# Performance work log

Hardware: AMD Instinct MI355X
Metric: run time of the kernel (lower is better)

The kernel has to match this reference:

```python
import jax, jax.numpy as jnp
import numpy as np
from jax import lax

B, L, M, H = 8, 16, 256, 53
HID, NH, HD = 64, 4, 16  # hidden_size, n_heads, head_dim
ACT = 15  # 3 sub-actions x 5 categories


def _lstm_last(x, Wih, Whh, bih, bhh):
    # x: [N, T, D] batch_first; torch LSTM gate order i,f,g,o. Returns last hidden [N, HID].
    N = x.shape[0]
    h0 = jnp.zeros((N, HID), x.dtype)
    c0 = jnp.zeros((N, HID), x.dtype)
    def step(carry, xt):
        h, c = carry
        g = xt @ Wih.T + bih + h @ Whh.T + bhh
        i, f, gg, o = jnp.split(g, 4, axis=-1)
        c = jax.nn.sigmoid(f) * c + jax.nn.sigmoid(i) * jnp.tanh(gg)
        h = jax.nn.sigmoid(o) * jnp.tanh(c)
        return (h, c), None
    (h, _), _ = lax.scan(step, (h0, c0), x.transpose(1, 0, 2))
    return h


def setup_inputs():
    key = jax.random.key(0)
    ks = jax.random.split(key, 32)
    rn = lambda k, sh: (jax.random.normal(k, sh, jnp.float32) * 0.05)
    Gmat = jax.random.randint(ks[3], (M, M), 0, 2)
    Gmat = Gmat.at[jnp.arange(M), jnp.arange(M)].set(1)  # self-contact so no all-masked row
    return {
        'x_actor': jax.random.normal(ks[0], (B, L, M, H), jnp.float32),
        'x_critic': jax.random.normal(ks[1], (B, L, M, H), jnp.float32),
        'action': jax.random.randint(ks[2], (B, M, 3), 0, 5),
        'Gmat': Gmat,
        'Wa': rn(ks[4], (HID, H)), 'ba': jnp.zeros((HID,), jnp.float32),
        'Wg': rn(ks[5], (HID, H)), 'bg': jnp.zeros((HID,), jnp.float32),
        'Qw': rn(ks[6], (HID, HID)), 'Kw': rn(ks[7], (HID, HID)),
        'W2': rn(ks[8], (HID, 2 * HID)), 'b2': jnp.zeros((HID,), jnp.float32),
        'Wih_a': rn(ks[9], (4 * HID, HID)), 'Whh_a': rn(ks[10], (4 * HID, HID)),
        'bih_a': jnp.zeros((4 * HID,), jnp.float32), 'bhh_a': jnp.zeros((4 * HID,), jnp.float32),
        'Wih_c': rn(ks[11], (4 * HID, HID)), 'Whh_c': rn(ks[12], (4 * HID, HID)),
        'bih_c': jnp.zeros((4 * HID,), jnp.float32), 'bhh_c': jnp.zeros((4 * HID,), jnp.float32),
        'Wma1': rn(ks[13], (HID, HID)), 'bma1': jnp.zeros((HID,), jnp.float32),
        'Wma2': rn(ks[14], (ACT, HID)), 'bma2': jnp.zeros((ACT,), jnp.float32),
        'Wmc1': rn(ks[15], (HID, HID)), 'bmc1': jnp.zeros((HID,), jnp.float32),
        'Wmc2': rn(ks[16], (1, HID)), 'bmc2': jnp.zeros((1,), jnp.float32),
    }


def reference(x_actor, x_critic, action, Gmat, Wa, ba, Wg, bg, Qw, Kw, W2, b2,
              Wih_a, Whh_a, bih_a, bhh_a, Wih_c, Whh_c, bih_c, bhh_c,
              Wma1, bma1, Wma2, bma2, Wmc1, bmc1, Wmc2, bmc2):
    Bb, Ll, Mm, Hh = x_actor.shape
    xa = x_actor.transpose(1, 0, 2, 3).reshape(Ll * Bb, Mm, Hh)
    xc = xa  # original code overwrites x_critic with x_actor (preserved)
    a_lin = xa @ Wa.T + ba                               # [LB, M, HID]
    # --- GAT (GCN2) ---
    s = xc @ Wg.T + bg                                   # [LB, M, HID]
    q = (s @ Qw).reshape(-1, Mm, NH, HD)
    k = (s @ Kw).reshape(-1, Mm, NH, HD)
    s4 = s.reshape(-1, Mm, NH, HD)
    att = jnp.einsum('blhe,bshe->bhls', q, k) / jnp.asarray(128.0, s.dtype) ** 0.5
    att = jnp.where(Gmat > 0, att, jnp.asarray(-9e15, att.dtype))
    att = jax.nn.softmax(att, axis=-1)
    s_out = jnp.einsum('bshe,bhls->blhe', s4, att).reshape(-1, Mm, NH * HD)
    c_feat = jnp.concatenate([s, s_out], axis=-1) @ W2.T + b2  # [LB, M, HID]
    # --- to sequences [B*M, L, HID] ---
    xa_seq = a_lin.reshape(Ll, Bb * Mm, HID).transpose(1, 0, 2)
    xc_seq = c_feat.reshape(Ll, Bb * Mm, HID).transpose(1, 0, 2)
    ah = _lstm_last(xa_seq, Wih_a, Whh_a, bih_a, bhh_a)          # [B*M, HID]
    ch = _lstm_last(xc_seq, Wih_c, Whh_c, bih_c, bhh_c).reshape(Bb, Mm, HID)
    logits = (jnp.tanh(ah @ Wma1.T + bma1) @ Wma2.T + bma2).reshape(Bb, Mm, 3, 5)
    logp = jax.nn.log_softmax(logits, axis=-1)
    lp = jnp.take_along_axis(logp, action[..., None], axis=-1).squeeze(-1)  # [B,M,3]
    ent = -jnp.sum(jnp.exp(logp) * logp, axis=-1)                           # [B,M,3]
    value = jnp.tanh(ch @ Wmc1.T + bmc1) @ Wmc2.T + bmc2                    # [B,M,1]
    return (action, lp.sum(-1), ent.sum(-1), value)
```

## Files before the change

kernel.cpp:

```cpp
#include <hip/hip_runtime.h>
#include <math.h>

#define B_ 8
#define L_ 16
#define M_ 256
#define H_ 53
#define HID_ 64
#define LB_ 128
#define SCALE_ 0.08838834764831845f

typedef __attribute__((ext_vector_type(8))) short bf16x8;
typedef __attribute__((ext_vector_type(4))) float f32x4;

__device__ inline unsigned short f2bf(float f) {
  unsigned u = __builtin_bit_cast(unsigned, f);
  unsigned r = (u + 0x7FFFu + ((u >> 16) & 1u)) >> 16;
  return (unsigned short)r;
}
__device__ inline float bf2f(unsigned short u) {
  unsigned v = ((unsigned)u) << 16;
  return __builtin_bit_cast(float, v);
}
__device__ inline float sigm(float x) { return __builtin_amdgcn_rcpf(1.f + __expf(-x)); }
__device__ inline float ftanh(float x) { return 1.f - 2.f * __builtin_amdgcn_rcpf(1.f + __expf(2.f * x)); }

__global__ __launch_bounds__(256) void kP_pre(
    const float* __restrict__ Wg, const float* __restrict__ bg,
    const float* __restrict__ Qw, const float* __restrict__ Kw,
    unsigned short* __restrict__ WQ_b, unsigned short* __restrict__ WK_b,
    float* __restrict__ bqk) {
  int blk = blockIdx.x, tid = threadIdx.x;
  if (blk < 32) {
    int idx = blk * 256 + tid;
    int which = idx >> 12, n = (idx >> 6) & 63, j = idx & 63;
    const float* Mm = which ? Kw : Qw;
    float acc = 0.f;
    if (j < 53) {
      for (int e = 0; e < 64; ++e) acc = fmaf(Mm[e * 64 + n], Wg[e * 53 + j], acc);
      if (which == 0) acc *= SCALE_;
    }
    (which ? WK_b : WQ_b)[n * 64 + j] = f2bf(acc);
  } else {
    if (tid < 128) {
      int which = tid >> 6, n = tid & 63;
      const float* Mm = which ? Kw : Qw;
      float acc = 0.f;
      for (int e = 0; e < 64; ++e) acc = fmaf(bg[e], Mm[e * 64 + n], acc);
      if (which == 0) acc *= SCALE_;
      bqk[tid] = acc;
    }
  }
}

#define XS 68
#define WS 68
#define OS 268
__global__ __launch_bounds__(256, 2) void kA_lin(const float* __restrict__ x,
    const float* __restrict__ Wa, const float* __restrict__ ba,
    const float* __restrict__ Wg, const float* __restrict__ bg,
    const unsigned short* __restrict__ WQ_b, const unsigned short* __restrict__ WK_b,
    const float* __restrict__ bqk,
    const int* __restrict__ Gmat, const float* __restrict__ Wih_c,
    const float* __restrict__ W2, const float* __restrict__ b2,
    const float* __restrict__ Whh_a, const float* __restrict__ Whh_c,
    const float* __restrict__ Wih_a,
    unsigned short* __restrict__ a_lin_bf, unsigned short* __restrict__ s_b,
    unsigned short* __restrict__ q_b, unsigned short* __restrict__ k_b,
    unsigned short* __restrict__ sT_b,
    unsigned short* __restrict__ Wfold_b, float* __restrict__ bias_fold,
    unsigned* __restrict__ gmask,
    unsigned short* __restrict__ Whha_b, unsigned short* __restrict__ Whhc_b,
    unsigned short* __restrict__ Wiha_b) {
  int blk = blockIdx.x, tid = threadIdx.x;
  if (blk >= 512) {
    int b2k = blk - 512;
    if (b2k < 128) {
      int idx = b2k * 256 + tid;
      int n = idx >> 7, t = idx & 127;
      float acc = 0.f;
      for (int e = 0; e < 64; ++e) acc = fmaf(Wih_c[n * 64 + e], W2[e * 128 + t], acc);
      Wfold_b[idx] = f2bf(acc);
    } else if (b2k < 192) {
      int l = (b2k - 128) * 4 + (tid >> 6);
      int ln = tid & 63;
      #pragma unroll
      for (int c = 0; c < 4; ++c) {
        int gv = Gmat[l * 256 + c * 64 + ln];
        unsigned long long msk = __ballot(gv > 0);
        if (ln == 0) {
          gmask[l * 8 + c * 2] = (unsigned)msk;
          gmask[l * 8 + c * 2 + 1] = (unsigned)(msk >> 32);
        }
      }
    } else if (b2k == 192) {
      float acc = 0.f;
      for (int e = 0; e < 64; ++e) acc = fmaf(Wih_c[tid * 64 + e], b2[e], acc);
      bias_fold[tid] = acc;
    } else {
      int base = (b2k - 193) * 2048;
      #pragma unroll
      for (int k = 0; k < 8; ++k) {
        int idx = base + k * 256 + tid;
        if (idx < 16384) Whha_b[idx] = f2bf(Whh_a[idx]);
        else if (idx < 32768) Whhc_b[idx - 16384] = f2bf(Whh_c[idx - 16384]);
        else Wiha_b[idx - 32768] = f2bf(Wih_a[idx - 32768]);
      }
    }
    return;
  }
  __shared__ __attribute__((aligned(16))) unsigned short x_lds[64 * XS];
  __shared__ __attribute__((aligned(16))) unsigned short w_lds[256 * WS];
  __shared__ float bias_lds[256];
  __shared__ __attribute__((aligned(16))) unsigned short out_lds[64 * OS];
  int row0 = blk * 64;
  for (int i = tid; i < 64 * 64; i += 256) {
    int r = i >> 6, j = i & 63;
    int row = row0 + r;
    int lb = row >> 8, m = row & 255;
    int l = lb >> 3, b = lb & 7;
    float v = (j < 53) ? x[((b * L_ + l) * M_ + m) * H_ + j] : 0.f;
    x_lds[r * XS + j] = f2bf(v);
  }
  for (int i = tid; i < 64 * 64; i += 256) {
    int n = i >> 6, j = i & 63;
    w_lds[n * WS + j] = (j < 53) ? f2bf(Wa[n * 53 + j]) : 0;
    w_lds[(64 + n) * WS + j] = (j < 53) ? f2bf(Wg[n * 53 + j]) : 0;
    w_lds[(128 + n) * WS + j] = WQ_b[i];
    w_lds[(192 + n) * WS + j] = WK_b[i];
  }
  {
    float bv;
    if (tid < 64) bv = ba[tid];
    else if (tid < 128) bv = bg[tid - 64];
    else bv = bqk[tid - 128];
    bias_lds[tid] = bv;
  }
  __syncthreads();
  int lane = tid & 63, w = tid >> 6;
  int c16 = lane & 15, q4 = lane >> 4;
  bf16x8 a0 = *(const bf16x8*)&x_lds[(w * 16 + c16) * XS + q4 * 8];
  bf16x8 a1 = *(const bf16x8*)&x_lds[(w * 16 + c16) * XS + 32 + q4 * 8];
  #pragma unroll
  for (int nt = 0; nt < 16; ++nt) {
    bf16x8 b0 = *(const bf16x8*)&w_lds[(nt * 16 + c16) * WS + q4 * 8];
    bf16x8 b1 = *(const bf16x8*)&w_lds[(nt * 16 + c16) * WS + 32 + q4 * 8];
    float bs = bias_lds[nt * 16 + c16];
    f32x4 acc = {bs, bs, bs, bs};
    acc = __builtin_amdgcn_mfma_f32_16x16x32_bf16(a0, b0, acc, 0, 0, 0);
    acc = __builtin_amdgcn_mfma_f32_16x16x32_bf16(a1, b1, acc, 0, 0, 0);
    #pragma unroll
    for (int rr = 0; rr < 4; ++rr)
      out_lds[(w * 16 + q4 * 4 + rr) * OS + nt * 16 + c16] = f2bf(acc[rr]);
  }
  __syncthreads();
  for (int i = tid; i < 2048; i += 256) {
    int r = i >> 5, seg = i & 31;
    int which = seg >> 3, n8 = (seg & 7) * 8;
    uint4 v = *(const uint4*)&out_lds[r * OS + which * 64 + n8];
    unsigned short* dst = which == 0 ? a_lin_bf : which == 1 ? s_b : which == 2 ? q_b : k_b;
    *(uint4*)&dst[(row0 + r) * 64 + n8] = v;
  }
  int lbA = row0 >> 8, m0 = row0 & 255;
  for (int i = tid; i < 1024; i += 256) {
    int e = i >> 4, mc = i & 15;
    ushort4 v;
    v.x = out_lds[(mc * 4 + 0) * OS + 64 + e];
    v.y = out_lds[(mc * 4 + 1) * OS + 64 + e];
    v.z = out_lds[(mc * 4 + 2) * OS + 64 + e];
    v.w = out_lds[(mc * 4 + 3) * OS + 64 + e];
    *(ushort4*)&sT_b[(lbA * 64 + e) * 256 + m0 + mc * 4] = v;
  }
}

__global__ __launch_bounds__(512, 4) void kB_attn(
    const unsigned short* __restrict__ qb, const unsigned short* __restrict__ kb,
    const unsigned short* __restrict__ sT, const unsigned* __restrict__ gmask,
    unsigned short* __restrict__ so_b) {
  __shared__ __attribute__((aligned(16))) unsigned short k_lds[256 * 68];
  __shared__ __attribute__((aligned(16))) unsigned short sT_lds[64 * 280];
  int blk = blockIdx.x;
  int lb = blk >> 2;
  int l0 = (blk & 3) << 6;
  int tid = threadIdx.x;
  int kbase = lb * 256;
  for (int i = tid; i < 2048; i += 512) {
    int s = i >> 3, e8 = (i & 7) * 8;
    *(uint4*)&k_lds[s * 68 + e8] = *(const uint4*)(kb + (kbase + s) * 64 + e8);
  }
  for (int i = tid; i < 2048; i += 512) {
    int e = i >> 5, m8 = (i & 31) * 8;
    *(uint4*)&sT_lds[e * 280 + m8] = *(const uint4*)(sT + (lb * 64 + e) * 256 + m8);
  }
  int lane = tid & 63, w = tid >> 6;
  int c16 = lane & 15, q4 = lane >> 4;
  int lrow0 = (w >> 1) * 16;
  int h0 = (w & 1) * 2;
  int lrow = lb * 256 + l0 + lrow0;
  const bf16x8 z8 = {0, 0, 0, 0, 0, 0, 0, 0};
  bf16x8 bq[2];
  #pragma unroll
  for (int hp = 0; hp < 2; ++hp) {
    int h = h0 + hp;
    bq[hp] = (q4 < 2) ? *(const bf16x8*)(qb + (lrow + c16) * 64 + h * 16 + q4 * 8) : z8;
  }
  unsigned gwv[8];
  #pragma unroll
  for (int sp = 0; sp < 8; ++sp) gwv[sp] = gmask[(l0 + lrow0 + c16) * 8 + sp];
  __syncthreads();
  f32x4 accO[2];
  float sumh[2];
  #pragma unroll
  for (int hp = 0; hp < 2; ++hp) { accO[hp] = (f32x4){0.f, 0.f, 0.f, 0.f}; sumh[hp] = 0.f; }

  #pragma unroll
  for (int sp = 0; sp < 8; ++sp) {
    unsigned gw = gwv[sp];
    #pragma unroll
    for (int hp = 0; hp < 2; ++hp) {
      int h = h0 + hp;
      unsigned pk0A, pk1A, pk0B, pk1B;
      #pragma unroll
      for (int tp = 0; tp < 2; ++tp) {
        int t = sp * 2 + tp;
        bf16x8 ka = z8;
        if (q4 < 2) ka = *(const bf16x8*)&k_lds[(t * 16 + c16) * 68 + h * 16 + q4 * 8];
        f32x4 d = __builtin_amdgcn_mfma_f32_16x16x32_bf16(ka, bq[hp], (f32x4){0.f, 0.f, 0.f, 0.f}, 0, 0, 0);
        int bitbase = tp * 16 + q4 * 4;
        float p0 = ((gw >> (bitbase + 0)) & 1u) ? __expf(d[0]) : 0.f;
        float p1 = ((gw >> (bitbase + 1)) & 1u) ? __expf(d[1]) : 0.f;
        float p2 = ((gw >> (bitbase + 2)) & 1u) ? __expf(d[2]) : 0.f;
        float p3 = ((gw >> (bitbase + 3)) & 1u) ? __expf(d[3]) : 0.f;
        sumh[hp] += (p0 + p1) + (p2 + p3);
        unsigned lo = (unsigned)f2bf(p0) | ((unsigned)f2bf(p1) << 16);
        unsigned hi = (unsigned)f2bf(p2) | ((unsigned)f2bf(p3) << 16);
        if (tp == 0) { pk0A = lo; pk1A = hi; } else { pk0B = lo; pk1B = hi; }
      }
      int srcA = ((q4 & 1) * 2) * 16 + c16, srcB = srcA + 16;
      unsigned g0A = (unsigned)__shfl((int)pk0A, srcA);
      unsigned g1A = (unsigned)__shfl((int)pk1A, srcA);
      unsigned g2A = (unsigned)__shfl((int)pk0A, srcB);
      unsigned g3A = (unsigned)__shfl((int)pk1A, srcB);
      unsigned g0B = (unsigned)__shfl((int)pk0B, srcA);
      unsigned g1B = (unsigned)__shfl((int)pk1B, srcA);
      unsigned g2B = (unsigned)__shfl((int)pk0B, srcB);
      unsigned g3B = (unsigned)__shfl((int)pk1B, srcB);
      bool useB = (q4 >= 2);
      uint4 av;
      av.x = useB ? g0B : g0A;
      av.y = useB ? g1B : g1A;
      av.z = useB ? g2B : g2A;
      av.w = useB ? g3B : g3A;
      bf16x8 af = __builtin_bit_cast(bf16x8, av);
      bf16x8 bs = *(const bf16x8*)&sT_lds[(h * 16 + c16) * 280 + sp * 32 + q4 * 8];
      accO[hp] = __builtin_amdgcn_mfma_f32_16x16x32_bf16(af, bs, accO[hp], 0, 0, 0);
    }
  }
  #pragma unroll
  for (int hp = 0; hp < 2; ++hp) {
    int h = h0 + hp;
    float s = sumh[hp];
    s += __shfl_xor(s, 16);
    s += __shfl_xor(s, 32);
    #pragma unroll
    for (int r = 0; r < 4; ++r) {
      float sv = __shfl(s, q4 * 4 + r);
      float o = accO[hp][r] / sv;
      so_b[(lb * 256 + l0 + lrow0 + q4 * 4 + r) * 64 + h * 16 + c16] = f2bf(o);
    }
  }
}

__global__ __launch_bounds__(256, 1) void kR_lstm(
    const unsigned short* __restrict__ a_lin_bf,
    const unsigned short* __restrict__ s_b, const unsigned short* __restrict__ so_b,
    const unsigned short* __restrict__ Wfold_b, const float* __restrict__ bias_fold,
    const unsigned short* __restrict__ Wiha_b,
    const unsigned short* __restrict__ Whha_b, const unsigned short* __restrict__ Whhc_b,
    const float* __restrict__ bih_a, const float* __restrict__ bhh_a,
    const float* __restrict__ bih_c, const float* __restrict__ bhh_c,
    const int* __restrict__ action,
    const float* __restrict__ Wma1, const float* __restrict__ bma1,
    const float* __restrict__ Wma2, const float* __restrict__ bma2,
    const float* __restrict__ Wmc1, const float* __restrict__ bmc1,
    const float* __restrict__ Wmc2, const float* __restrict__ bmc2,
    float* __restrict__ out) {
  int blk = blockIdx.x;
  int which = blk >> 7, g = blk & 127;
  int seq0 = g * 16;
  int b = seq0 >> 8, m0 = seq0 & 255;
  __shared__ __attribute__((aligned(16))) unsigned short h_lds[2][16][72];
  __shared__ __attribute__((aligned(16))) unsigned short ha_lds[16][72];
  __shared__ float logit_lds[16][16];
  __shared__ float grp_lds[16][8];
  __shared__ float val_lds[16][4];
  int tid = threadIdx.x;
  int lane = tid & 63, w = tid >> 6;
  int c16 = lane & 15, q4 = lane >> 4;
  int hs0 = w * 16;
  const unsigned short* Whh_b = which ? Whhc_b : Whha_b;
  const float* bih = which ? bih_c : bih_a;
  const float* bhh = which ? bhh_c : bhh_a;
  bf16x8 bwhh[4][2];
  float bias[4];
  #pragma unroll
  for (int nt = 0; nt < 4; ++nt) {
    int n = nt * 64 + hs0 + c16;
    bias[nt] = bih[n] + bhh[n] + (which ? bias_fold[n] : 0.f);
    #pragma unroll
    for (int kf = 0; kf < 2; ++kf)
      bwhh[nt][kf] = *(const bf16x8*)(Whh_b + n * 64 + kf * 32 + q4 * 8);
  }
  for (int i = tid; i < 576; i += 256) ((unsigned*)h_lds)[i] = 0u;
  float cr[4] = {0.f, 0.f, 0.f, 0.f};
  const int STEP = 2048 * 64;
  __syncthreads();
  int cur = 0;
  if (which == 0) {
    bf16x8 bwin[4][2];
    #pragma unroll
    for (int nt = 0; nt < 4; ++nt) {
      int n = nt * 64 + hs0 + c16;
      #pragma unroll
      for (int kf = 0; kf < 2; ++kf)
        bwin[nt][kf] = *(const bf16x8*)(Wiha_b + n * 64 + kf * 32 + q4 * 8);
    }
    const unsigned short* inb = a_lin_bf + (b * 256 + m0 + c16) * 64;
    bf16x8 i0c = *(const bf16x8*)(inb + q4 * 8);
    bf16x8 i1c = *(const bf16x8*)(inb + 32 + q4 * 8);
    for (int l = 0; l < L_; ++l) {
      bf16x8 i0n = i0c, i1n = i1c;
      if (l < L_ - 1) {
        i0n = *(const bf16x8*)(inb + (l + 1) * STEP + q4 * 8);
        i1n = *(const bf16x8*)(inb + (l + 1) * STEP + 32 + q4 * 8);
      }
      bf16x8 ah0 = *(const bf16x8*)&h_lds[cur][c16][q4 * 8];
      bf16x8 ah1 = *(const bf16x8*)&h_lds[cur][c16][32 + q4 * 8];
      f32x4 acc[4];
      #pragma unroll
      for (int nt = 0; nt < 4; ++nt) {
        f32x4 a = {bias[nt], bias[nt], bias[nt], bias[nt]};
        a = __builtin_amdgcn_mfma_f32_16x16x32_bf16(i0c, bwin[nt][0], a, 0, 0, 0);
        a = __builtin_amdgcn_mfma_f32_16x16x32_bf16(i1c, bwin[nt][1], a, 0, 0, 0);
        a = __builtin_amdgcn_mfma_f32_16x16x32_bf16(ah0, bwhh[nt][0], a, 0, 0, 0);
        a = __builtin_amdgcn_mfma_f32_16x16x32_bf16(ah1, bwhh[nt][1], a, 0, 0, 0);
        acc[nt] = a;
      }
      #pragma unroll
      for (int rr = 0; rr < 4; ++rr) {
        float si = sigm(acc[0][rr]);
        float sf = sigm(acc[1][rr]);
        float gg = ftanh(acc[2][rr]);
        float so_ = sigm(acc[3][rr]);
        cr[rr] = sf * cr[rr] + si * gg;
        float hvv = so_ * ftanh(cr[rr]);
        h_lds[cur ^ 1][q4 * 4 + rr][hs0 + c16] = f2bf(hvv);
      }
      __syncthreads();
      cur ^= 1;
      i0c = i0n; i1c = i1n;
    }
  } else {
    bf16x8 bwf[4][4];
    #pragma unroll
    for (int nt = 0; nt < 4; ++nt) {
      int n = nt * 64 + hs0 + c16;
      #pragma unroll
      for (int kc = 0; kc < 4; ++kc)
        bwf[nt][kc] = *(const bf16x8*)(Wfold_b + n * 128 + kc * 32 + q4 * 8);
    }
    const unsigned short* sbB = s_b + (b * 256 + m0 + c16) * 64;
    const unsigned short* soB = so_b + (b * 256 + m0 + c16) * 64;
    bf16x8 s0c = *(const bf16x8*)(sbB + q4 * 8);
    bf16x8 s1c = *(const bf16x8*)(sbB + 32 + q4 * 8);
    bf16x8 o0c = *(const bf16x8*)(soB + q4 * 8);
    bf16x8 o1c = *(const bf16x8*)(soB + 32 + q4 * 8);
    for (int l = 0; l < L_; ++l) {
      bf16x8 s0n = s0c, s1n = s1c, o0n = o0c, o1n = o1c;
      if (l < L_ - 1) {
        s0n = *(const bf16x8*)(sbB + (l + 1) * STEP + q4 * 8);
        s1n = *(const bf16x8*)(sbB + (l + 1) * STEP + 32 + q4 * 8);
        o0n = *(const bf16x8*)(soB + (l + 1) * STEP + q4 * 8);
        o1n = *(const bf16x8*)(soB + (l + 1) * STEP + 32 + q4 * 8);
      }
      bf16x8 ah0 = *(const bf16x8*)&h_lds[cur][c16][q4 * 8];
      bf16x8 ah1 = *(const bf16x8*)&h_lds[cur][c16][32 + q4 * 8];
      f32x4 acc[4];
      #pragma unroll
      for (int nt = 0; nt < 4; ++nt) {
        f32x4 a = {bias[nt], bias[nt], bias[nt], bias[nt]};
        a = __builtin_amdgcn_mfma_f32_16x16x32_bf16(s0c, bwf[nt][0], a, 0, 0, 0);
        a = __builtin_amdgcn_mfma_f32_16x16x32_bf16(s1c, bwf[nt][1], a, 0, 0, 0);
        a = __builtin_amdgcn_mfma_f32_16x16x32_bf16(o0c, bwf[nt][2], a, 0, 0, 0);
        a = __builtin_amdgcn_mfma_f32_16x16x32_bf16(o1c, bwf[nt][3], a, 0, 0, 0);
        a = __builtin_amdgcn_mfma_f32_16x16x32_bf16(ah0, bwhh[nt][0], a, 0, 0, 0);
        a = __builtin_amdgcn_mfma_f32_16x16x32_bf16(ah1, bwhh[nt][1], a, 0, 0, 0);
        acc[nt] = a;
      }
      #pragma unroll
      for (int rr = 0; rr < 4; ++rr) {
        float si = sigm(acc[0][rr]);
        float sf = sigm(acc[1][rr]);
        float gg = ftanh(acc[2][rr]);
        float so_ = sigm(acc[3][rr]);
        cr[rr] = sf * cr[rr] + si * gg;
        float hvv = so_ * ftanh(cr[rr]);
        h_lds[cur ^ 1][q4 * 4 + rr][hs0 + c16] = f2bf(hvv);
      }
      __syncthreads();
      cur ^= 1;
      s0c = s0n; s1c = s1n; o0c = o0n; o1c = o1n;
    }
  }
  bf16x8 fh0 = *(const bf16x8*)&h_lds[cur][c16][q4 * 8];
  bf16x8 fh1 = *(const bf16x8*)&h_lds[cur][c16][32 + q4 * 8];
  if (which == 0) {
    bf16x8 bm1[2];
    #pragma unroll
    for (int kf = 0; kf < 2; ++kf) {
      const float* wp = Wma1 + (hs0 + c16) * 64 + kf * 32 + q4 * 8;
      bf16x8 bb;
      #pragma unroll
      for (int j = 0; j < 8; ++j) bb[j] = (short)f2bf(wp[j]);
      bm1[kf] = bb;
    }
    float bs = bma1[hs0 + c16];
    f32x4 acc = {bs, bs, bs, bs};
    acc = __builtin_amdgcn_mfma_f32_16x16x32_bf16(fh0, bm1[0], acc, 0, 0, 0);
    acc = __builtin_amdgcn_mfma_f32_16x16x32_bf16(fh1, bm1[1], acc, 0, 0, 0);
    #pragma unroll
    for (int rr = 0; rr < 4; ++rr)
      ha_lds[q4 * 4 + rr][hs0 + c16] = f2bf(ftanh(acc[rr]));
    __syncthreads();
    if (w == 0) {
      bf16x8 af0 = *(const bf16x8*)&ha_lds[c16][q4 * 8];
      bf16x8 af1 = *(const bf16x8*)&ha_lds[c16][32 + q4 * 8];
      const bf16x8 z8 = {0, 0, 0, 0, 0, 0, 0, 0};
      bf16x8 bw2[2] = {z8, z8};
      float bs2 = 0.f;
      if (c16 < 15) {
        #pragma unroll
        for (int kf = 0; kf < 2; ++kf) {
          const float* wp = Wma2 + c16 * 64 + kf * 32 + q4 * 8;
          bf16x8 bb;
          #pragma unroll
          for (int j = 0; j < 8; ++j) bb[j] = (short)f2bf(wp[j]);
          bw2[kf] = bb;
        }
        bs2 = bma2[c16];
      }
      f32x4 acc2 = {bs2, bs2, bs2, bs2};
      acc2 = __builtin_amdgcn_mfma_f32_16x16x32_bf16(af0, bw2[0], acc2, 0, 0, 0);
      acc2 = __builtin_amdgcn_mfma_f32_16x16x32_bf16(af1, bw2[1], acc2, 0, 0, 0);
      #pragma unroll
      for (int rr = 0; rr < 4; ++rr)
        logit_lds[q4 * 4 + rr][c16] = acc2[rr];
    }
    __syncthreads();
    if (tid < 48) {
      int useq = tid & 15, t = tid >> 4;
      int n = seq0 + useq;
      float l0 = logit_lds[useq][t * 5 + 0], l1 = logit_lds[useq][t * 5 + 1];
      float l2 = logit_lds[useq][t * 5 + 2], l3 = logit_lds[useq][t * 5 + 3];
      float l4 = logit_lds[useq][t * 5 + 4];
      float mx = fmaxf(fmaxf(fmaxf(l0, l1), fmaxf(l2, l3)), l4);
      float sm = __expf(l0 - mx) + __expf(l1 - mx) + __expf(l2 - mx) +
                 __expf(l3 - mx) + __expf(l4 - mx);
      float lse = __logf(sm) + mx;
      int a = action[n * 3 + t];
      float lp0 = l0 - lse, lp1 = l1 - lse, lp2 = l2 - lse, lp3 = l3 - lse, lp4 = l4 - lse;
      float lpsel = logit_lds[useq][t * 5 + a] - lse;
      float ent = -(__expf(lp0) * lp0 + __expf(lp1) * lp1 + __expf(lp2) * lp2 +
                    __expf(lp3) * lp3 + __expf(lp4) * lp4);
      grp_lds[useq][t] = lpsel;
      grp_lds[useq][4 + t] = ent;
      out[n * 3 + t] = (float)a;
    }
    __syncthreads();
    if (tid < 16) {
      int n = seq0 + tid;
      out[6144 + n] = grp_lds[tid][0] + grp_lds[tid][1] + grp_lds[tid][2];
      out[8192 + n] = grp_lds[tid][4] + grp_lds[tid][5] + grp_lds[tid][6];
    }
  } else {
    bf16x8 bm1[2];
    #pragma unroll
    for (int kf = 0; kf < 2; ++kf) {
      const float* wp = Wmc1 + (hs0 + c16) * 64 + kf * 32 + q4 * 8;
      bf16x8 bb;
      #pragma unroll
      for (int j = 0; j < 8; ++j) bb[j] = (short)f2bf(wp[j]);
      bm1[kf] = bb;
    }
    float bs = bmc1[hs0 + c16];
    f32x4 acc = {bs, bs, bs, bs};
    acc = __builtin_amdgcn_mfma_f32_16x16x32_bf16(fh0, bm1[0], acc, 0, 0, 0);
    acc = __builtin_amdgcn_mfma_f32_16x16x32_bf16(fh1, bm1[1], acc, 0, 0, 0);
    float wv2 = Wmc2[hs0 + c16];
    float pv[4];
    #pragma unroll
    for (int rr = 0; rr < 4; ++rr) pv[rr] = ftanh(acc[rr]) * wv2;
    #pragma unroll
    for (int rr = 0; rr < 4; ++rr) {
      pv[rr] += __shfl_xor(pv[rr], 1);
      pv[rr] += __shfl_xor(pv[rr], 2);
      pv[rr] += __shfl_xor(pv[rr], 4);
      pv[rr] += __shfl_xor(pv[rr], 8);
    }
    if (c16 == 0) {
      #pragma unroll
      for (int rr = 0; rr < 4; ++rr) val_lds[q4 * 4 + rr][w] = pv[rr];
    }
    __syncthreads();
    if (tid < 16) {
      int n = seq0 + tid;
      out[10240 + n] = val_lds[tid][0] + val_lds[tid][1] + val_lds[tid][2] +
                       val_lds[tid][3] + bmc2[0];
    }
  }
}

extern "C" void kernel_launch(void* const* d_in, const int* in_sizes, int n_in,
                              void* d_out, int out_size, void* d_ws, size_t ws_size,
                              hipStream_t stream) {
  const float* x_actor = (const float*)d_in[0];
  const int* action = (const int*)d_in[2];
  const int* Gmat  = (const int*)d_in[3];
  const float* Wa = (const float*)d_in[4];  const float* ba = (const float*)d_in[5];
  const float* Wg = (const float*)d_in[6];  const float* bg = (const float*)d_in[7];
  const float* Qw = (const float*)d_in[8];  const float* Kw = (const float*)d_in[9];
  const float* W2 = (const float*)d_in[10]; const float* b2 = (const float*)d_in[11];
  const float* Wih_a = (const float*)d_in[12]; const float* Whh_a = (const float*)d_in[13];
  const float* bih_a = (const float*)d_in[14]; const float* bhh_a = (const float*)d_in[15];
  const float* Wih_c = (const float*)d_in[16]; const float* Whh_c = (const float*)d_in[17];
  const float* bih_c = (const float*)d_in[18]; const float* bhh_c = (const float*)d_in[19];
  const float* Wma1 = (const float*)d_in[20]; const float* bma1 = (const float*)d_in[21];
  const float* Wma2 = (const float*)d_in[22]; const float* bma2 = (const float*)d_in[23];
  const float* Wmc1 = (const float*)d_in[24]; const float* bmc1 = (const float*)d_in[25];
  const float* Wmc2 = (const float*)d_in[26]; const float* bmc2 = (const float*)d_in[27];

  unsigned short* us = (unsigned short*)d_ws;
  unsigned short* a_lin_bf = us;
  unsigned short* s_b  = us + 2097152;
  unsigned short* q_b  = us + 4194304;
  unsigned short* k_b  = us + 6291456;
  unsigned short* sT_b = us + 8388608;
  unsigned short* so_b = us + 10485760;
  unsigned short* Wfold_b = us + 12582912;
  unsigned short* Whha_b  = us + 12615680;
  unsigned short* Whhc_b  = us + 12632064;
  unsigned short* Wiha_b  = us + 12648448;
  unsigned short* WQ_b    = us + 12664832;
  unsigned short* WK_b    = us + 12668928;
  float* fb = (float*)(us + 12673024);
  float* bias_fold = fb;
  float* bqk = fb + 256;
  unsigned* gmask = (unsigned*)(fb + 384);
  float* out = (float*)d_out;

  kP_pre<<<33, 256, 0, stream>>>(Wg, bg, Qw, Kw, WQ_b, WK_b, bqk);
  kA_lin<<<729, 256, 0, stream>>>(x_actor, Wa, ba, Wg, bg, WQ_b, WK_b, bqk,
                                  Gmat, Wih_c, W2, b2, Whh_a, Whh_c, Wih_a,
                                  a_lin_bf, s_b, q_b, k_b, sT_b,
                                  Wfold_b, bias_fold, gmask,
                                  Whha_b, Whhc_b, Wiha_b);
  kB_attn<<<512, 512, 0, stream>>>(q_b, k_b, sT_b, gmask, so_b);
  kR_lstm<<<256, 256, 0, stream>>>(a_lin_bf, s_b, so_b, Wfold_b, bias_fold,
                                   Wiha_b, Whha_b, Whhc_b,
                                   bih_a, bhh_a, bih_c, bhh_c,
                                   action, Wma1, bma1, Wma2, bma2,
                                   Wmc1, bmc1, Wmc2, bmc2, out);
}
```

Baseline: 73.87 us.

## Precompute LSTM input projections for all timesteps before the recurrent loop

Hoists the input-to-hidden MFMA products for all 16 timesteps out of the recurrence into a register array, so the serial loop only runs the hidden-to-hidden MFMAs, gate math and barrier. This shortens the latency-critical dependent chain per step and lets all global loads issue up front. The cost is a 16x4 f32x4 accumulator array (256 VGPRs per lane), which risks spilling or lower occupancy.

```diff
diff --git a/kernel.cpp b/kernel.cpp
--- a/kernel.cpp
+++ b/kernel.cpp
@@ -314,7 +314,8 @@
   float cr[4] = {0.f, 0.f, 0.f, 0.f};
   const int STEP = 2048 * 64;
   __syncthreads();
-  int cur = 0;
+
+  f32x4 accin[L_][4];
   if (which == 0) {
     bf16x8 bwin[4][2];
     #pragma unroll
@@ -325,39 +326,17 @@
         bwin[nt][kf] = *(const bf16x8*)(Wiha_b + n * 64 + kf * 32 + q4 * 8);
     }
     const unsigned short* inb = a_lin_bf + (b * 256 + m0 + c16) * 64;
-    bf16x8 i0c = *(const bf16x8*)(inb + q4 * 8);
-    bf16x8 i1c = *(const bf16x8*)(inb + 32 + q4 * 8);
+    #pragma unroll
     for (int l = 0; l < L_; ++l) {
-      bf16x8 i0n = i0c, i1n = i1c;
-      if (l < L_ - 1) {
-        i0n = *(const bf16x8*)(inb + (l + 1) * STEP + q4 * 8);
-        i1n = *(const bf16x8*)(inb + (l + 1) * STEP + 32 + q4 * 8);
-      }
-      bf16x8 ah0 = *(const bf16x8*)&h_lds[cur][c16][q4 * 8];
-      bf16x8 ah1 = *(const bf16x8*)&h_lds[cur][c16][32 + q4 * 8];
-      f32x4 acc[4];
+      bf16x8 i0 = *(const bf16x8*)(inb + l * STEP + q4 * 8);
+      bf16x8 i1 = *(const bf16x8*)(inb + l * STEP + 32 + q4 * 8);
       #pragma unroll
       for (int nt = 0; nt < 4; ++nt) {
         f32x4 a = {bias[nt], bias[nt], bias[nt], bias[nt]};
-        a = __builtin_amdgcn_mfma_f32_16x16x32_bf16(i0c, bwin[nt][0], a, 0, 0, 0);
-        a = __builtin_amdgcn_mfma_f32_16x16x32_bf16(i1c, bwin[nt][1], a, 0, 0, 0);
-        a = __builtin_amdgcn_mfma_f32_16x16x32_bf16(ah0, bwhh[nt][0], a, 0, 0, 0);
-        a = __builtin_amdgcn_mfma_f32_16x16x32_bf16(ah1, bwhh[nt][1], a, 0, 0, 0);
-        acc[nt] = a;
+        a = __builtin_amdgcn_mfma_f32_16x16x32_bf16(i0, bwin[nt][0], a, 0, 0, 0);
+        a = __builtin_amdgcn_mfma_f32_16x16x32_bf16(i1, bwin[nt][1], a, 0, 0, 0);
+        accin[l][nt] = a;
       }
-      #pragma unroll
-      for (int rr = 0; rr < 4; ++rr) {
-        float si = sigm(acc[0][rr]);
-        float sf = sigm(acc[1][rr]);
-        float gg = ftanh(acc[2][rr]);
-        float so_ = sigm(acc[3][rr]);
-        cr[rr] = sf * cr[rr] + si * gg;
-        float hvv = so_ * ftanh(cr[rr]);
-        h_lds[cur ^ 1][q4 * 4 + rr][hs0 + c16] = f2bf(hvv);
-      }
-      __syncthreads();
-      cur ^= 1;
-      i0c = i0n; i1c = i1n;
     }
   } else {
     bf16x8 bwf[4][4];
@@ -370,47 +349,51 @@
     }
     const unsigned short* sbB = s_b + (b * 256 + m0 + c16) * 64;
     const unsigned short* soB = so_b + (b * 256 + m0 + c16) * 64;
-    bf16x8 s0c = *(const bf16x8*)(sbB + q4 * 8);
-    bf16x8 s1c = *(const bf16x8*)(sbB + 32 + q4 * 8);
-    bf16x8 o0c = *(const bf16x8*)(soB + q4 * 8);
-    bf16x8 o1c = *(const bf16x8*)(soB + 32 + q4 * 8);
+    #pragma unroll
     for (int l = 0; l < L_; ++l) {
-      bf16x8 s0n = s0c, s1n = s1c, o0n = o0c, o1n = o1c;
-      if (l < L_ - 1) {
-        s0n = *(const bf16x8*)(sbB + (l + 1) * STEP + q4 * 8);
-        s1n = *(const bf16x8*)(sbB + (l + 1) * STEP + 32 + q4 * 8);
-        o0n = *(const bf16x8*)(soB + (l + 1) * STEP + q4 * 8);
-        o1n = *(const bf16x8*)(soB + (l + 1) * STEP + 32 + q4 * 8);
-      }
-      bf16x8 ah0 = *(const bf16x8*)&h_lds[cur][c16][q4 * 8];
-      bf16x8 ah1 = *(const bf16x8*)&h_lds[cur][c16][32 + q4 * 8];
-      f32x4 acc[4];
+      bf16x8 s0 = *(const bf16x8*)(sbB + l * STEP + q4 * 8);
+      bf16x8 s1 = *(const bf16x8*)(sbB + l * STEP + 32 + q4 * 8);
+      bf16x8 o0 = *(const bf16x8*)(soB + l * STEP + q4 * 8);
+      bf16x8 o1 = *(const bf16x8*)(soB + l * STEP + 32 + q4 * 8);
       #pragma unroll
       for (int nt = 0; nt < 4; ++nt) {
         f32x4 a = {bias[nt], bias[nt], bias[nt], bias[nt]};
-        a = __builtin_amdgcn_mfma_f32_16x16x32_bf16(s0c, bwf[nt][0], a, 0, 0, 0);
-        a = __builtin_amdgcn_mfma_f32_16x16x32_bf16(s1c, bwf[nt][1], a, 0, 0, 0);
-        a = __builtin_amdgcn_mfma_f32_16x16x32_bf16(o0c, bwf[nt][2], a, 0, 0, 0);
-        a = __builtin_amdgcn_mfma_f32_16x16x32_bf16(o1c, bwf[nt][3], a, 0, 0, 0);
-        a = __builtin_amdgcn_mfma_f32_16x16x32_bf16(ah0, bwhh[nt][0], a, 0, 0, 0);
-        a = __builtin_amdgcn_mfma_f32_16x16x32_bf16(ah1, bwhh[nt][1], a, 0, 0, 0);
-        acc[nt] = a;
+        a = __builtin_amdgcn_mfma_f32_16x16x32_bf16(s0, bwf[nt][0], a, 0, 0, 0);
+        a = __builtin_amdgcn_mfma_f32_16x16x32_bf16(s1, bwf[nt][1], a, 0, 0, 0);
+        a = __builtin_amdgcn_mfma_f32_16x16x32_bf16(o0, bwf[nt][2], a, 0, 0, 0);
+        a = __builtin_amdgcn_mfma_f32_16x16x32_bf16(o1, bwf[nt][3], a, 0, 0, 0);
+        accin[l][nt] = a;
       }
-      #pragma unroll
-      for (int rr = 0; rr < 4; ++rr) {
-        float si = sigm(acc[0][rr]);
-        float sf = sigm(acc[1][rr]);
-        float gg = ftanh(acc[2][rr]);
-        float so_ = sigm(acc[3][rr]);
-        cr[rr] = sf * cr[rr] + si * gg;
-        float hvv = so_ * ftanh(cr[rr]);
-        h_lds[cur ^ 1][q4 * 4 + rr][hs0 + c16] = f2bf(hvv);
-      }
-      __syncthreads();
-      cur ^= 1;
-      s0c = s0n; s1c = s1n; o0c = o0n; o1c = o1n;
-    }
-  }
+    }
+  }
+
+  int cur = 0;
+  #pragma unroll
+  for (int l = 0; l < L_; ++l) {
+    bf16x8 ah0 = *(const bf16x8*)&h_lds[cur][c16][q4 * 8];
+    bf16x8 ah1 = *(const bf16x8*)&h_lds[cur][c16][32 + q4 * 8];
+    f32x4 acc[4];
+    #pragma unroll
+    for (int nt = 0; nt < 4; ++nt) {
+      f32x4 a = accin[l][nt];
+      a = __builtin_amdgcn_mfma_f32_16x16x32_bf16(ah0, bwhh[nt][0], a, 0, 0, 0);
+      a = __builtin_amdgcn_mfma_f32_16x16x32_bf16(ah1, bwhh[nt][1], a, 0, 0, 0);
+      acc[nt] = a;
+    }
+    #pragma unroll
+    for (int rr = 0; rr < 4; ++rr) {
+      float si = sigm(acc[0][rr]);
+      float sf = sigm(acc[1][rr]);
+      float gg = ftanh(acc[2][rr]);
+      float so_ = sigm(acc[3][rr]);
+      cr[rr] = sf * cr[rr] + si * gg;
+      float hvv = so_ * ftanh(cr[rr]);
+      h_lds[cur ^ 1][q4 * 4 + rr][hs0 + c16] = f2bf(hvv);
+    }
+    __syncthreads();
+    cur ^= 1;
+  }
+
   bf16x8 fh0 = *(const bf16x8*)&h_lds[cur][c16][q4 * 8];
   bf16x8 fh1 = *(const bf16x8*)&h_lds[cur][c16][32 + q4 * 8];
   if (which == 0) {
```

Result: slower. 76.98 us (+4.2%).

## Move weight prep into pre-kernel and coalesce x tile loads in kA_lin

Applied to the files above, without the earlier changes.

All weight preparation (Wfold, gmask, bias_fold, bf16 copies of the LSTM weights, and a new pre-converted bf16 Wa/Wg buffer) moves from extra blocks of kA_lin into kP_pre, so kA_lin launches only its 512 GEMM blocks. kA_lin now loads each 64-row x tile as one contiguous float block with 16-byte vector loads into a reused shared buffer, then converts it to bf16 MFMA fragments in registers, instead of doing strided scalar gathers. Weights are copied into LDS with vector loads of the pre-converted bf16 data. The cost is a larger kP_pre launch that runs serially before kA_lin, plus an extra barrier and more LDS traffic for the fp32 staging.

```diff
diff --git a/kernel.cpp b/kernel.cpp
--- a/kernel.cpp
+++ b/kernel.cpp
@@ -25,10 +25,18 @@
 __device__ inline float ftanh(float x) { return 1.f - 2.f * __builtin_amdgcn_rcpf(1.f + __expf(2.f * x)); }
 
 __global__ __launch_bounds__(256) void kP_pre(
-    const float* __restrict__ Wg, const float* __restrict__ bg,
+    const float* __restrict__ Wa, const float* __restrict__ Wg,
+    const float* __restrict__ bg,
     const float* __restrict__ Qw, const float* __restrict__ Kw,
+    const int* __restrict__ Gmat, const float* __restrict__ Wih_c,
+    const float* __restrict__ W2, const float* __restrict__ b2,
+    const float* __restrict__ Whh_a, const float* __restrict__ Whh_c,
+    const float* __restrict__ Wih_a,
     unsigned short* __restrict__ WQ_b, unsigned short* __restrict__ WK_b,
-    float* __restrict__ bqk) {
+    float* __restrict__ bqk, unsigned short* __restrict__ Wfold_b,
+    float* __restrict__ bias_fold, unsigned* __restrict__ gmask,
+    unsigned short* __restrict__ Whha_b, unsigned short* __restrict__ Whhc_b,
+    unsigned short* __restrict__ Wiha_b, unsigned short* __restrict__ Wab_b) {
   int blk = blockIdx.x, tid = threadIdx.x;
   if (blk < 32) {
     int idx = blk * 256 + tid;
@@ -40,7 +48,7 @@
       if (which == 0) acc *= SCALE_;
     }
     (which ? WK_b : WQ_b)[n * 64 + j] = f2bf(acc);
-  } else {
+  } else if (blk == 32) {
     if (tid < 128) {
       int which = tid >> 6, n = tid & 63;
       const float* Mm = which ? Kw : Qw;
@@ -49,84 +57,84 @@
       if (which == 0) acc *= SCALE_;
       bqk[tid] = acc;
     }
-  }
-}
-
-#define XS 68
+    float bacc = 0.f;
+    for (int e = 0; e < 64; ++e) bacc = fmaf(Wih_c[tid * 64 + e], b2[e], bacc);
+    bias_fold[tid] = bacc;
+  } else if (blk < 97) {
+    int l = (blk - 33) * 4 + (tid >> 6);
+    int ln = tid & 63;
+    #pragma unroll
+    for (int c = 0; c < 4; ++c) {
+      int gv = Gmat[l * 256 + c * 64 + ln];
+      unsigned long long msk = __ballot(gv > 0);
+      if (ln == 0) {
+        gmask[l * 8 + c * 2] = (unsigned)msk;
+        gmask[l * 8 + c * 2 + 1] = (unsigned)(msk >> 32);
+      }
+    }
+  } else if (blk < 225) {
+    int idx = (blk - 97) * 256 + tid;
+    int n = idx >> 7, t = idx & 127;
+    float acc = 0.f;
+    for (int e = 0; e < 64; ++e) acc = fmaf(Wih_c[n * 64 + e], W2[e * 128 + t], acc);
+    Wfold_b[idx] = f2bf(acc);
+  } else if (blk < 249) {
+    int base = (blk - 225) * 2048;
+    #pragma unroll
+    for (int k = 0; k < 8; ++k) {
+      int idx = base + k * 256 + tid;
+      if (idx < 16384) Whha_b[idx] = f2bf(Whh_a[idx]);
+      else if (idx < 32768) Whhc_b[idx - 16384] = f2bf(Whh_c[idx - 16384]);
+      else Wiha_b[idx - 32768] = f2bf(Wih_a[idx - 32768]);
+    }
+  } else {
+    int base = (blk - 249) * 4096;
+    #pragma unroll
+    for (int k = 0; k < 16; ++k) {
+      int idx = base + k * 256 + tid;
+      int n = idx >> 6, j = idx & 63;
+      float v = 0.f;
+      if (j < 53) v = (n < 64) ? Wa[n * 53 + j] : Wg[(n - 64) * 53 + j];
+      Wab_b[idx] = f2bf(v);
+    }
+  }
+}
+
 #define WS 68
 #define OS 268
 __global__ __launch_bounds__(256, 2) void kA_lin(const float* __restrict__ x,
-    const float* __restrict__ Wa, const float* __restrict__ ba,
-    const float* __restrict__ Wg, const float* __restrict__ bg,
+    const unsigned short* __restrict__ Wab_b,
     const unsigned short* __restrict__ WQ_b, const unsigned short* __restrict__ WK_b,
+    const float* __restrict__ ba, const float* __restrict__ bg,
     const float* __restrict__ bqk,
-    const int* __restrict__ Gmat, const float* __restrict__ Wih_c,
-    const float* __restrict__ W2, const float* __restrict__ b2,
-    const float* __restrict__ Whh_a, const float* __restrict__ Whh_c,
-    const float* __restrict__ Wih_a,
     unsigned short* __restrict__ a_lin_bf, unsigned short* __restrict__ s_b,
     unsigned short* __restrict__ q_b, unsigned short* __restrict__ k_b,
-    unsigned short* __restrict__ sT_b,
-    unsigned short* __restrict__ Wfold_b, float* __restrict__ bias_fold,
-    unsigned* __restrict__ gmask,
-    unsigned short* __restrict__ Whha_b, unsigned short* __restrict__ Whhc_b,
-    unsigned short* __restrict__ Wiha_b) {
-  int blk = blockIdx.x, tid = threadIdx.x;
-  if (blk >= 512) {
-    int b2k = blk - 512;
-    if (b2k < 128) {
-      int idx = b2k * 256 + tid;
-      int n = idx >> 7, t = idx & 127;
-      float acc = 0.f;
-      for (int e = 0; e < 64; ++e) acc = fmaf(Wih_c[n * 64 + e], W2[e * 128 + t], acc);
-      Wfold_b[idx] = f2bf(acc);
-    } else if (b2k < 192) {
-      int l = (b2k - 128) * 4 + (tid >> 6);
-      int ln = tid & 63;
-      #pragma unroll
-      for (int c = 0; c < 4; ++c) {
-        int gv = Gmat[l * 256 + c * 64 + ln];
-        unsigned long long msk = __ballot(gv > 0);
-        if (ln == 0) {
-          gmask[l * 8 + c * 2] = (unsigned)msk;
-          gmask[l * 8 + c * 2 + 1] = (unsigned)(msk >> 32);
-        }
-      }
-    } else if (b2k == 192) {
-      float acc = 0.f;
-      for (int e = 0; e < 64; ++e) acc = fmaf(Wih_c[tid * 64 + e], b2[e], acc);
-      bias_fold[tid] = acc;
-    } else {
-      int base = (b2k - 193) * 2048;
-      #pragma unroll
-      for (int k = 0; k < 8; ++k) {
-        int idx = base + k * 256 + tid;
-        if (idx < 16384) Whha_b[idx] = f2bf(Whh_a[idx]);
-        else if (idx < 32768) Whhc_b[idx - 16384] = f2bf(Whh_c[idx - 16384]);
-        else Wiha_b[idx - 32768] = f2bf(Wih_a[idx - 32768]);
-      }
-    }
-    return;
-  }
-  __shared__ __attribute__((aligned(16))) unsigned short x_lds[64 * XS];
-  __shared__ __attribute__((aligned(16))) unsigned short w_lds[256 * WS];
-  __shared__ float bias_lds[256];
-  __shared__ __attribute__((aligned(16))) unsigned short out_lds[64 * OS];
+    unsigned short* __restrict__ sT_b) {
+  __shared__ __attribute__((aligned(16))) char smem[70144];
+  float* x_raw = (float*)smem;
+  unsigned short* out_lds = (unsigned short*)smem;
+  unsigned short* w_lds = (unsigned short*)(smem + 34304);
+  float* bias_lds = (float*)(smem + 69120);
+  int tid = threadIdx.x, blk = blockIdx.x;
   int row0 = blk * 64;
-  for (int i = tid; i < 64 * 64; i += 256) {
-    int r = i >> 6, j = i & 63;
-    int row = row0 + r;
-    int lb = row >> 8, m = row & 255;
-    int l = lb >> 3, b = lb & 7;
-    float v = (j < 53) ? x[((b * L_ + l) * M_ + m) * H_ + j] : 0.f;
-    x_lds[r * XS + j] = f2bf(v);
-  }
-  for (int i = tid; i < 64 * 64; i += 256) {
-    int n = i >> 6, j = i & 63;
-    w_lds[n * WS + j] = (j < 53) ? f2bf(Wa[n * 53 + j]) : 0;
-    w_lds[(64 + n) * WS + j] = (j < 53) ? f2bf(Wg[n * 53 + j]) : 0;
-    w_lds[(128 + n) * WS + j] = WQ_b[i];
-    w_lds[(192 + n) * WS + j] = WK_b[i];
+  int lbA = row0 >> 8, m0 = row0 & 255;
+  int lA = lbA >> 3, bA = lbA & 7;
+  {
+    const uint4* xs = (const uint4*)(x + ((bA * L_ + lA) * M_ + m0) * H_);
+    uint4* xr = (uint4*)x_raw;
+    #pragma unroll
+    for (int k = 0; k < 4; ++k) {
+      int i = k * 256 + tid;
+      if (i < 848) xr[i] = xs[i];
+    }
+  }
+  #pragma unroll
+  for (int k = 0; k < 8; ++k) {
+    int i = k * 256 + tid;
+    int n = i >> 3, c8 = (i & 7) * 8;
+    const unsigned short* src = n < 128 ? Wab_b + n * 64
+                              : (n < 192 ? WQ_b + (n - 128) * 64 : WK_b + (n - 192) * 64);
+    *(uint4*)&w_lds[n * WS + c8] = *(const uint4*)(src + c8);
   }
   {
     float bv;
@@ -138,8 +146,17 @@
   __syncthreads();
   int lane = tid & 63, w = tid >> 6;
   int c16 = lane & 15, q4 = lane >> 4;
-  bf16x8 a0 = *(const bf16x8*)&x_lds[(w * 16 + c16) * XS + q4 * 8];
-  bf16x8 a1 = *(const bf16x8*)&x_lds[(w * 16 + c16) * XS + 32 + q4 * 8];
+  int lrow = w * 16 + c16;
+  bf16x8 a0, a1;
+  #pragma unroll
+  for (int e = 0; e < 8; ++e)
+    a0[e] = (short)f2bf(x_raw[lrow * H_ + q4 * 8 + e]);
+  #pragma unroll
+  for (int e = 0; e < 8; ++e) {
+    int c = 32 + q4 * 8 + e;
+    a1[e] = (c < H_) ? (short)f2bf(x_raw[lrow * H_ + c]) : (short)0;
+  }
+  __syncthreads();
   #pragma unroll
   for (int nt = 0; nt < 16; ++nt) {
     bf16x8 b0 = *(const bf16x8*)&w_lds[(nt * 16 + c16) * WS + q4 * 8];
@@ -153,15 +170,18 @@
       out_lds[(w * 16 + q4 * 4 + rr) * OS + nt * 16 + c16] = f2bf(acc[rr]);
   }
   __syncthreads();
-  for (int i = tid; i < 2048; i += 256) {
+  #pragma unroll
+  for (int k = 0; k < 8; ++k) {
+    int i = k * 256 + tid;
     int r = i >> 5, seg = i & 31;
     int which = seg >> 3, n8 = (seg & 7) * 8;
     uint4 v = *(const uint4*)&out_lds[r * OS + which * 64 + n8];
     unsigned short* dst = which == 0 ? a_lin_bf : which == 1 ? s_b : which == 2 ? q_b : k_b;
     *(uint4*)&dst[(row0 + r) * 64 + n8] = v;
   }
-  int lbA = row0 >> 8, m0 = row0 & 255;
-  for (int i = tid; i < 1024; i += 256) {
+  #pragma unroll
+  for (int k = 0; k < 4; ++k) {
+    int i = k * 256 + tid;
     int e = i >> 4, mc = i & 15;
     ushort4 v;
     v.x = out_lds[(mc * 4 + 0) * OS + 64 + e];
@@ -551,18 +571,19 @@
   unsigned short* Wiha_b  = us + 12648448;
   unsigned short* WQ_b    = us + 12664832;
   unsigned short* WK_b    = us + 12668928;
-  float* fb = (float*)(us + 12673024);
+  unsigned short* Wab_b   = us + 12673024;
+  float* fb = (float*)(us + 12681216);
   float* bias_fold = fb;
   float* bqk = fb + 256;
   unsigned* gmask = (unsigned*)(fb + 384);
   float* out = (float*)d_out;
 
-  kP_pre<<<33, 256, 0, stream>>>(Wg, bg, Qw, Kw, WQ_b, WK_b, bqk);
-  kA_lin<<<729, 256, 0, stream>>>(x_actor, Wa, ba, Wg, bg, WQ_b, WK_b, bqk,
-                                  Gmat, Wih_c, W2, b2, Whh_a, Whh_c, Wih_a,
-                                  a_lin_bf, s_b, q_b, k_b, sT_b,
-                                  Wfold_b, bias_fold, gmask,
-                                  Whha_b, Whhc_b, Wiha_b);
+  kP_pre<<<251, 256, 0, stream>>>(Wa, Wg, bg, Qw, Kw, Gmat, Wih_c, W2, b2,
+                                  Whh_a, Whh_c, Wih_a,
+                                  WQ_b, WK_b, bqk, Wfold_b, bias_fold, gmask,
+                                  Whha_b, Whhc_b, Wiha_b, Wab_b);
+  kA_lin<<<512, 256, 0, stream>>>(x_actor, Wab_b, WQ_b, WK_b, ba, bg, bqk,
+                                  a_lin_bf, s_b, q_b, k_b, sT_b);
   kB_attn<<<512, 512, 0, stream>>>(q_b, k_b, sT_b, gmask, so_b);
   kR_lstm<<<256, 256, 0, stream>>>(a_lin_bf, s_b, so_b, Wfold_b, bias_fold,
                                    Wiha_b, Whha_b, Whhc_b,
```

Result: faster. 68.59 us (-7.1%).
